# Kernel tuning notes

Hardware: AMD Instinct MI355X
Metric: run time of the kernel (lower is better)

Reference implementation:

```python
import jax, jax.numpy as jnp
import numpy as np


def setup_inputs() -> dict:
    key = jax.random.key(0)
    k1, k2, k3 = jax.random.split(key, 3)
    B, N, D = 8, 4096, 64
    q = jax.random.normal(k1, (B, N, D), dtype=jnp.float32)
    k = jax.random.normal(k2, (B, N, D), dtype=jnp.float32)
    v = jax.random.normal(k3, (B, N, D), dtype=jnp.float32)
    attn_mask = jnp.ones((B, N), dtype=jnp.int32)  # 1 = attend, 0 = padding
    return {"q": q, "k": k, "v": v, "attn_mask": attn_mask}


def reference(q, k, v, attn_mask):
    # q: [B, n_q, d], k/v: [B, n_k, d], attn_mask: [B, n_k]
    d = q.shape[-1]
    n_q, n_k = q.shape[1], k.shape[1]
    scale = jnp.sqrt(jnp.asarray(d, dtype=q.dtype))
    # [B, n_q, n_k] attention logits
    logits = jnp.einsum("bqd,bkd->bqk", q, k) / scale
    # causal (mask_future=True): tril keep-mask over (n_q, n_k)
    causal = jnp.tril(jnp.ones((n_q, n_k), dtype=bool))
    neg_inf = jnp.asarray(-jnp.inf, dtype=logits.dtype)
    logits = jnp.where(causal[None, :, :], logits, neg_inf)
    # padding mask broadcast over query dim: [B, 1, n_k]
    logits = jnp.where(attn_mask[:, None, :] == 0, neg_inf, logits)
    w = jax.nn.softmax(logits, axis=-1)
    return jnp.einsum("bqk,bkd->bqd", w, v)
```

## Files before the change

### kernel.cpp

```cpp
#include <hip/hip_runtime.h>


#define BATCH 8
#define SEQ   4096
#define DIM   64
#define QT    64
#define NKT   (SEQ / 64)

typedef __attribute__((ext_vector_type(8))) short bf16x8;
typedef __attribute__((ext_vector_type(4))) float f32x4;
typedef __attribute__((ext_vector_type(4))) unsigned u32x4;

__device__ inline short f2bf(float f) {
    unsigned u = __builtin_bit_cast(unsigned, f);
    u += 0x7FFFu + ((u >> 16) & 1u);
    return (short)(u >> 16);
}

__device__ inline unsigned pk2bf(float a, float b) {
    unsigned ua = __builtin_bit_cast(unsigned, a) + 0x8000u;
    unsigned ub = __builtin_bit_cast(unsigned, b) + 0x8000u;
    return __builtin_amdgcn_perm(ub, ua, 0x07060302u);
}

__device__ inline float fast_exp2(float x) {
#if __has_builtin(__builtin_amdgcn_exp2f)
    return __builtin_amdgcn_exp2f(x);
#else
    return exp2f(x);
#endif
}

__device__ inline void gl_lds16(const void* g, void* l) {
    __builtin_amdgcn_global_load_lds(
        (const __attribute__((address_space(1))) void*)g,
        (__attribute__((address_space(3))) void*)l, 16, 0, 0);
}

__device__ inline f32x4 ntl4(const float* p) {
    return __builtin_nontemporal_load((const f32x4*)p);
}

__global__ __launch_bounds__(256)
void prep_kv(const float* __restrict__ kg, const float* __restrict__ vg,
             const int* __restrict__ mg, short* __restrict__ kw,
             short* __restrict__ vw, float* __restrict__ mf) {
    const int tile = blockIdx.x;
    const float* kp = kg + (size_t)tile * 64 * DIM;
    const float* vp = vg + (size_t)tile * 64 * DIM;
    short* ko = kw + (size_t)tile * 4096;
    short* vo = vw + (size_t)tile * 4096;
    const int t = threadIdx.x;
    if (mf && t < 64) {
        const int* mp = mg + (size_t)tile * 64;
        mf[(size_t)tile * 64 + t] = mp[t] ? 0.0f : -1e30f;
    }
#pragma unroll
    for (int i = 0; i < 4; ++i) {
        const int flat = i * 256 + t;
        const int key = flat >> 4, d0 = (flat & 15) * 4;
        const f32x4 kv = ntl4(kp + (size_t)key * DIM + d0);
        uint2 kpk;
        kpk.x = pk2bf(kv[0], kv[1]); kpk.y = pk2bf(kv[2], kv[3]);
        *(uint2*)(ko + (((d0 >> 3) << 6) + key) * 8 + (d0 & 7)) = kpk;
        const f32x4 vv = ntl4(vp + (size_t)key * DIM + d0);
        const int vcell = ((key >> 5) << 2) | ((key >> 2) & 3);
        const int vj    = (((key >> 4) & 1) << 2) | (key & 3);
        vo[((vcell << 6) + d0 + 0) * 8 + vj] = f2bf(vv[0]);
        vo[((vcell << 6) + d0 + 1) * 8 + vj] = f2bf(vv[1]);
        vo[((vcell << 6) + d0 + 2) * 8 + vj] = f2bf(vv[2]);
        vo[((vcell << 6) + d0 + 3) * 8 + vj] = f2bf(vv[3]);
    }
}

__global__ __launch_bounds__(256, 4)
void attn_split4(const float* __restrict__ qg, float* __restrict__ og,
                 const short* __restrict__ kw, const short* __restrict__ vw,
                 const float* __restrict__ mf, float* __restrict__ opart,
                 float* __restrict__ lpart) {
    __shared__ __align__(16) char smem[32768];
    short* KbS = (short*)smem;
    float* OX = (float*)smem;
    float* LB = (float*)(smem + 16384);

    const int t    = threadIdx.x;
    const int w    = t >> 6;
    const int L    = t & 63;
    const int c15  = L & 15;
    const int quad = L >> 4;
    const int qgrp = w >> 1;
    const int kh   = w & 1;

    const int id  = blockIdx.x;
    const int b   = id & 7;
    const int r_  = id >> 3;
    const int j   = r_ & 31;
    const int ch  = r_ >> 5;
    const int nL  = 64 - j;
    const int qLt = 63 - j;

    const float* qp  = qg + (size_t)b * SEQ * DIM;
    const float* mb  = mf + (size_t)b * SEQ;
    const short* kwb = kw + (size_t)b * NKT * 4096;
    const short* vwb = vw + (size_t)b * NKT * 4096;
    float* osl = opart + (size_t)(b * 32 + j) * 12288;
    float* lsl = lpart + (size_t)(b * 32 + j) * 384;
    const float qscale = 0.125f * 1.44269504088896340736f;

    auto stage = [&](int bs, int kt) {
        const short* ks = kwb + (size_t)kt * 4096;
        const short* vs = vwb + (size_t)kt * 4096;
        const int off = w << 10;
        short* base = KbS + bs * 8192;
        gl_lds16(ks + off +       (L << 3), base + off);
        gl_lds16(ks + off + 512 + (L << 3), base + off + 512);
        gl_lds16(vs + off +       (L << 3), base + 4096 + off);
        gl_lds16(vs + off + 512 + (L << 3), base + 4096 + off + 512);
    };

    bf16x8 vones;
#pragma unroll
    for (int z = 0; z < 8; ++z) vones[z] = (short)0x3F80;

    int sqt[2], sk0[2], sk1[2], smode[2], sos[2], sls[2], nseg;
    sos[0] = sos[1] = 0; sls[0] = sls[1] = 0;
    if (ch == 0) {
        nseg = 1;
        sqt[0] = qLt; sk0[0] = 0;  sk1[0] = 16; smode[0] = 0; sls[0] = 0;
    } else if (ch == 1) {
        nseg = 1;
        sqt[0] = qLt; sk0[0] = 16; sk1[0] = 32; smode[0] = 1; sos[0] = 0; sls[0] = 1;
    } else if (ch == 2) {
        if (nL >= 48) {
            nseg = 1;
            sqt[0] = qLt; sk0[0] = 32; sk1[0] = 48; smode[0] = 1; sos[0] = 1; sls[0] = 2;
        } else {
            nseg = 2;
            sqt[0] = qLt; sk0[0] = 32; sk1[0] = nL;      smode[0] = 1; sos[0] = 1; sls[0] = 2;
            sqt[1] = j;   sk0[1] = 0;  sk1[1] = 48 - nL; smode[1] = 0; sls[1] = 4;
        }
    } else {
        if (nL > 48) {
            nseg = 2;
            sqt[0] = qLt; sk0[0] = 48; sk1[0] = nL;    smode[0] = 1; sos[0] = 2; sls[0] = 3;
            sqt[1] = j;   sk0[1] = 0;  sk1[1] = j + 1; smode[1] = 2;
        } else if (nL == 48) {
            nseg = 1;
            sqt[0] = j; sk0[0] = 0; sk1[0] = j + 1; smode[0] = 2;
        } else {
            nseg = 1;
            sqt[0] = j; sk0[0] = 48 - nL; sk1[0] = j + 1; smode[0] = 1; sos[0] = 2; sls[0] = 5;
        }
    }

    for (int seg = 0; seg < nseg; ++seg) {
        const int qt   = sqt[seg];
        const int kt0  = sk0[seg];
        const int kt1  = sk1[seg];
        const int mode = smode[seg];

        const int qbase = qt * QT;
        int qrow[2];
        qrow[0] = qbase + qgrp * 32 + c15;
        qrow[1] = qrow[0] + 16;

        bf16x8 Qf[2][2];
#pragma unroll
        for (int s = 0; s < 2; ++s) {
#pragma unroll
            for (int c = 0; c < 2; ++c) {
                const float* src = qp + (size_t)qrow[s] * DIM + c * 32 + quad * 8;
                float4 x = *(const float4*)(src);
                float4 y = *(const float4*)(src + 4);
                bf16x8 f;
                f[0] = f2bf(x.x * qscale); f[1] = f2bf(x.y * qscale);
                f[2] = f2bf(x.z * qscale); f[3] = f2bf(x.w * qscale);
                f[4] = f2bf(y.x * qscale); f[5] = f2bf(y.y * qscale);
                f[6] = f2bf(y.z * qscale); f[7] = f2bf(y.w * qscale);
                Qf[s][c] = f;
            }
        }
        asm volatile("" ::: "memory");

        f32x4 lacc[2];
        lacc[0] = (f32x4){0.f, 0.f, 0.f, 0.f};
        lacc[1] = (f32x4){0.f, 0.f, 0.f, 0.f};
        f32x4 Oacc[2][4];
#pragma unroll
        for (int s = 0; s < 2; ++s)
#pragma unroll
            for (int nb = 0; nb < 4; ++nb)
                Oacc[s][nb] = (f32x4){0.f, 0.f, 0.f, 0.f};

        stage(0, kt0);
        int cur = 0;
        const float* mrow = mb + (size_t)kt0 * 64 + (2 * kh) * 16 + quad * 4;

        for (int kt = kt0; kt < kt1; ++kt) {
            asm volatile("s_waitcnt vmcnt(0)" ::: "memory");
            __builtin_amdgcn_s_barrier();
            asm volatile("" ::: "memory");

            const float4 ma0 = *(const float4*)(mrow);
            const float4 ma1 = *(const float4*)(mrow + 16);
            mrow += 64;
            asm volatile("" ::: "memory");
            if (kt + 1 < kt1) stage(cur ^ 1, kt + 1);

            const short* Kt = KbS + cur * 8192;
            const short* Vt = Kt + 4096;
            cur ^= 1;

            f32x4 sacc[2][2];
#pragma unroll
            for (int s = 0; s < 2; ++s) {
                sacc[s][0] = (f32x4){ma0.x, ma0.y, ma0.z, ma0.w};
                sacc[s][1] = (f32x4){ma1.x, ma1.y, ma1.z, ma1.w};
            }
            __builtin_amdgcn_s_setprio(1);
#pragma unroll
            for (int c = 0; c < 2; ++c) {
#pragma unroll
                for (int i = 0; i < 2; ++i) {
                    bf16x8 kf = *(const bf16x8*)&Kt[(((quad + 4 * c) << 6) + (2 * kh + i) * 16 + c15) * 8];
#pragma unroll
                    for (int s = 0; s < 2; ++s)
                        sacc[s][i] = __builtin_amdgcn_mfma_f32_16x16x32_bf16(kf, Qf[s][c], sacc[s][i], 0, 0, 0);
                }
            }
            __builtin_amdgcn_s_setprio(0);

            const bool diag = (kt == qt);
            bf16x8 pf[2];
#pragma unroll
            for (int s = 0; s < 2; ++s) {
                unsigned pu[4];
#pragma unroll
                for (int i = 0; i < 2; ++i) {
                    float p[4];
#pragma unroll
                    for (int r = 0; r < 4; ++r) {
                        float sv = sacc[s][i][r];
                        if (diag) {
                            const int keyg = kt * 64 + (2 * kh + i) * 16 + quad * 4 + r;
                            if (keyg > qrow[s]) sv = -1e30f;
                        }
                        p[r] = fast_exp2(sv);
                    }
                    pu[2 * i]     = pk2bf(p[0], p[1]);
                    pu[2 * i + 1] = pk2bf(p[2], p[3]);
                }
                pf[s] = __builtin_bit_cast(bf16x8,
                    (u32x4){pu[0], pu[1], pu[2], pu[3]});
            }

            __builtin_amdgcn_s_setprio(1);
#pragma unroll
            for (int nb = 0; nb < 4; ++nb) {
                bf16x8 vf = *(const bf16x8*)&Vt[(((kh * 4 + quad) << 6) + nb * 16 + c15) * 8];
#pragma unroll
                for (int s = 0; s < 2; ++s)
                    Oacc[s][nb] = __builtin_amdgcn_mfma_f32_16x16x32_bf16(pf[s], vf, Oacc[s][nb], 0, 0, 0);
            }
            lacc[0] = __builtin_amdgcn_mfma_f32_16x16x32_bf16(pf[0], vones, lacc[0], 0, 0, 0);
            lacc[1] = __builtin_amdgcn_mfma_f32_16x16x32_bf16(pf[1], vones, lacc[1], 0, 0, 0);
            __builtin_amdgcn_s_setprio(0);
        }

        __syncthreads();
        if (kh == 1) {
#pragma unroll
            for (int s = 0; s < 2; ++s) {
#pragma unroll
                for (int r = 0; r < 4; ++r) {
                    const int rl = qgrp * 32 + s * 16 + quad * 4 + r;
#pragma unroll
                    for (int nb = 0; nb < 4; ++nb)
                        OX[rl * 64 + nb * 16 + c15] = Oacc[s][nb][r];
                    if (c15 == 0) LB[rl] = lacc[s][r];
                }
            }
        }
        __syncthreads();
        if (kh == 0) {
            float* dst = (mode == 1) ? osl + (size_t)sos[seg] * 4096
                                     : og + ((size_t)b * SEQ + qbase) * DIM;
#pragma unroll
            for (int s = 0; s < 2; ++s) {
#pragma unroll
                for (int r = 0; r < 4; ++r) {
                    const int rl = qgrp * 32 + s * 16 + quad * 4 + r;
                    const float lt = lacc[s][r] + LB[rl];
                    const float ir = (mode == 2) ? 1.0f / lt : 1.0f;
                    if (mode != 2 && c15 == 0)
                        lsl[sls[seg] * 64 + rl] = lt;
#pragma unroll
                    for (int nb = 0; nb < 4; ++nb)
                        dst[(size_t)rl * DIM + nb * 16 + c15] =
                            (Oacc[s][nb][r] + OX[rl * 64 + nb * 16 + c15]) * ir;
                }
            }
        }
        __syncthreads();
    }
}

__global__ __launch_bounds__(256)
void merge4(float* __restrict__ og, const float* __restrict__ opart,
            const float* __restrict__ lpart) {
    const int id = blockIdx.x;
    const int b = id & 7, j = id >> 3;
    const int nL = 64 - j, qLt = 63 - j;
    const float* os = opart + (size_t)(b * 32 + j) * 12288;
    const float* ls = lpart + (size_t)(b * 32 + j) * 384;
    const int t = threadIdx.x;
    const bool has3 = (nL > 48);

    float* opL = og + ((size_t)b * SEQ + (size_t)qLt * 64) * DIM;
#pragma unroll
    for (int i = 0; i < 4; ++i) {
        const int flat = i * 256 + t;
        const int row = flat >> 4;
        const int c4  = (flat & 15) * 4;
        float l = ls[row] + ls[64 + row] + ls[128 + row];
        if (has3) l += ls[192 + row];
        const float inv = 1.0f / l;
        const float4 a  = *(const float4*)(opL + (size_t)row * DIM + c4);
        const float4 p0 = *(const float4*)(os + (size_t)row * 64 + c4);
        const float4 p1 = *(const float4*)(os + 4096 + (size_t)row * 64 + c4);
        float sx = a.x + p0.x + p1.x;
        float sy = a.y + p0.y + p1.y;
        float sz = a.z + p0.z + p1.z;
        float sw = a.w + p0.w + p1.w;
        if (has3) {
            const float4 p2 = *(const float4*)(os + 8192 + (size_t)row * 64 + c4);
            sx += p2.x; sy += p2.y; sz += p2.z; sw += p2.w;
        }
        float4 r;
        r.x = sx * inv; r.y = sy * inv; r.z = sz * inv; r.w = sw * inv;
        *(float4*)(opL + (size_t)row * DIM + c4) = r;
    }

    if (nL < 48) {
        float* opS = og + ((size_t)b * SEQ + (size_t)j * 64) * DIM;
#pragma unroll
        for (int i = 0; i < 4; ++i) {
            const int flat = i * 256 + t;
            const int row = flat >> 4;
            const int c4  = (flat & 15) * 4;
            const float inv = 1.0f / (ls[256 + row] + ls[320 + row]);
            const float4 a  = *(const float4*)(opS + (size_t)row * DIM + c4);
            const float4 p2 = *(const float4*)(os + 8192 + (size_t)row * 64 + c4);
            float4 r;
            r.x = (a.x + p2.x) * inv;
            r.y = (a.y + p2.y) * inv;
            r.z = (a.z + p2.z) * inv;
            r.w = (a.w + p2.w) * inv;
            *(float4*)(opS + (size_t)row * DIM + c4) = r;
        }
    }
}

template <bool WS>
__global__ __launch_bounds__(512, 4)
void attn_fwd(const float* __restrict__ qg, const float* __restrict__ kg,
              const float* __restrict__ vg, const int* __restrict__ mg,
              float* __restrict__ og, const short* __restrict__ kw,
              const short* __restrict__ vw) {
    __shared__ __align__(16) char smem[59392];
    short* KbS = (short*)smem;
    short* VbS = (short*)(smem + 16384);
    float* Ml  = (float*)(smem + 43008);
    float* OX = (float*)smem;
    float* LB = (float*)(smem + 16384);

    const int t    = threadIdx.x;
    const int w    = t >> 6;
    const int L    = t & 63;
    const int c15  = L & 15;
    const int quad = L >> 4;
    const int qsub = w & 3;
    const int kh   = w >> 2;

    const int id = blockIdx.x;
    const int b  = id & 7;
    const int j  = id >> 3;
    const int qb = (j < 32) ? (63 - j) : (j - 32);
    const int qbase  = qb * QT;
    const int ntiles = qb + 1;

    const float* qp = qg + (size_t)b * SEQ * DIM;
    const float* kp = kg + (size_t)b * SEQ * DIM;
    const float* vp = vg + (size_t)b * SEQ * DIM;
    const int*   mp = mg + (size_t)b * SEQ;
    const short* kwb = WS ? kw + (size_t)b * NKT * 4096 : nullptr;
    const short* vwb = WS ? vw + (size_t)b * NKT * 4096 : nullptr;

    const int qrow = qbase + qsub * 16 + c15;
    const float qscale = 0.125f * 1.44269504088896340736f;

    bf16x8 Qf[2];
#pragma unroll
    for (int c = 0; c < 2; ++c) {
        const float* src = qp + (size_t)qrow * DIM + c * 32 + quad * 8;
        float4 x = *(const float4*)(src);
        float4 y = *(const float4*)(src + 4);
        bf16x8 f;
        f[0] = f2bf(x.x * qscale); f[1] = f2bf(x.y * qscale);
        f[2] = f2bf(x.z * qscale); f[3] = f2bf(x.w * qscale);
        f[4] = f2bf(y.x * qscale); f[5] = f2bf(y.y * qscale);
        f[6] = f2bf(y.z * qscale); f[7] = f2bf(y.w * qscale);
        Qf[c] = f;
    }

    auto stage = [&](int bs, int kt) {
        const short* ks = kwb + (size_t)kt * 4096;
        const short* vs = vwb + (size_t)kt * 4096;
        const int off = w << 9;
        gl_lds16(ks + off + (L << 3), KbS + bs * 4096 + off);
        gl_lds16(vs + off + (L << 3), VbS + bs * 4096 + off);
    };

    for (int i = t; i < ntiles * 64; i += 512)
        Ml[i] = mp[i] ? 0.0f : -1e30f;

    float lsum = 0.0f;
    f32x4 Oacc[4];
#pragma unroll
    for (int nb = 0; nb < 4; ++nb) Oacc[nb] = (f32x4){0.f, 0.f, 0.f, 0.f};

    if constexpr (WS) stage(0, 0);

    for (int kt = 0; kt < ntiles; ++kt) {
        const int cur = WS ? (kt & 1) : 0;

        if constexpr (!WS) {
            __syncthreads();
#pragma unroll
            for (int it = 0; it < 2; ++it) {
                const int flat = it * 512 + t;
                const int key = flat >> 4, d0 = (flat & 15) * 4;
                const float4 kv = *(const float4*)(kp + (size_t)(kt * 64 + key) * DIM + d0);
                uint2 kk;
                kk.x = pk2bf(kv.x, kv.y); kk.y = pk2bf(kv.z, kv.w);
                *(uint2*)&KbS[(((d0 >> 3) << 6) + key) * 8 + (d0 & 7)] = kk;
                const float4 vv = *(const float4*)(vp + (size_t)(kt * 64 + key) * DIM + d0);
                const int vcell = ((key >> 5) << 2) | ((key >> 2) & 3);
                const int vj    = (((key >> 4) & 1) << 2) | (key & 3);
                VbS[((vcell << 6) + d0 + 0) * 8 + vj] = f2bf(vv.x);
                VbS[((vcell << 6) + d0 + 1) * 8 + vj] = f2bf(vv.y);
                VbS[((vcell << 6) + d0 + 2) * 8 + vj] = f2bf(vv.z);
                VbS[((vcell << 6) + d0 + 3) * 8 + vj] = f2bf(vv.w);
            }
            __syncthreads();
        } else {
            __syncthreads();
            if (kt + 1 < ntiles) stage(cur ^ 1, kt + 1);
        }

        const short* Kt = KbS + cur * 4096;
        const short* Vt = VbS + cur * 4096;

        f32x4 sacc[2];
        sacc[0] = (f32x4){0.f, 0.f, 0.f, 0.f};
        sacc[1] = (f32x4){0.f, 0.f, 0.f, 0.f};
#pragma unroll
        for (int c = 0; c < 2; ++c) {
#pragma unroll
            for (int i = 0; i < 2; ++i) {
                bf16x8 kf = *(const bf16x8*)&Kt[(((quad + 4 * c) << 6) + (2 * kh + i) * 16 + c15) * 8];
                sacc[i] = __builtin_amdgcn_mfma_f32_16x16x32_bf16(kf, Qf[c], sacc[i], 0, 0, 0);
            }
        }

        const bool diag = (kt == ntiles - 1);
        unsigned pu[4];
#pragma unroll
        for (int i = 0; i < 2; ++i) {
            const int kb = 2 * kh + i;
            const float4 ma = *(const float4*)&Ml[kt * 64 + kb * 16 + quad * 4];
            const float mar[4] = {ma.x, ma.y, ma.z, ma.w};
            float p[4];
#pragma unroll
            for (int r = 0; r < 4; ++r) {
                float s = sacc[i][r] + mar[r];
                if (diag) {
                    const int keyg = kt * 64 + kb * 16 + quad * 4 + r;
                    if (keyg > qrow) s = -1e30f;
                }
                p[r] = fast_exp2(fminf(s, 80.0f));
                lsum += p[r];
            }
            pu[2 * i]     = pk2bf(p[0], p[1]);
            pu[2 * i + 1] = pk2bf(p[2], p[3]);
        }

        const bf16x8 pf = __builtin_bit_cast(bf16x8,
            (u32x4){pu[0], pu[1], pu[2], pu[3]});
#pragma unroll
        for (int nb = 0; nb < 4; ++nb) {
            bf16x8 vf = *(const bf16x8*)&Vt[(((kh * 4 + quad) << 6) + nb * 16 + c15) * 8];
            Oacc[nb] = __builtin_amdgcn_mfma_f32_16x16x32_bf16(pf, vf, Oacc[nb], 0, 0, 0);
        }
    }

    lsum += __shfl_xor(lsum, 16);
    lsum += __shfl_xor(lsum, 32);

    __syncthreads();
    if (w >= 4) {
        const int g = w & 3;
#pragma unroll
        for (int r = 0; r < 4; ++r) {
            const int q = quad * 4 + r;
#pragma unroll
            for (int nb = 0; nb < 4; ++nb)
                OX[(g * 16 + q) * 64 + nb * 16 + c15] = Oacc[nb][r];
        }
        if (quad == 0) LB[g * 16 + c15] = lsum;
    }
    __syncthreads();
    if (w < 4) {
        const float inv = 1.0f / (lsum + LB[w * 16 + c15]);
        float* op = og + (size_t)b * SEQ * DIM;
#pragma unroll
        for (int r = 0; r < 4; ++r) {
            const float ir = __shfl(inv, (L & 48) + ((L & 48) >> 2) + r);
            const int row = qbase + w * 16 + quad * 4 + r;
#pragma unroll
            for (int nb = 0; nb < 4; ++nb)
                op[(size_t)row * DIM + nb * 16 + c15] =
                    (Oacc[nb][r] + OX[(w * 16 + quad * 4 + r) * 64 + nb * 16 + c15]) * ir;
        }
    }
}

extern "C" void kernel_launch(void* const* d_in, const int* in_sizes, int n_in,
                              void* d_out, int out_size, void* d_ws, size_t ws_size,
                              hipStream_t stream) {
    (void)in_sizes; (void)n_in; (void)out_size;
    const float* q = (const float*)d_in[0];
    const float* k = (const float*)d_in[1];
    const float* v = (const float*)d_in[2];
    const int*   m = (const int*)d_in[3];
    float* o = (float*)d_out;

    const size_t kvB    = (size_t)BATCH * NKT * 4096 * sizeof(short);
    const size_t maddB  = (size_t)BATCH * SEQ * sizeof(float);
    const size_t opartB = (size_t)BATCH * 32 * 12288 * sizeof(float);
    const size_t lpartB = (size_t)BATCH * 32 * 384 * sizeof(float);
    const size_t need4  = 2 * kvB + maddB + opartB + lpartB;

    if (ws_size >= need4) {
        short* kw = (short*)d_ws;
        short* vw = kw + (size_t)BATCH * NKT * 4096;
        float* mf = (float*)((char*)d_ws + 2 * kvB);
        float* opart = (float*)((char*)d_ws + 2 * kvB + maddB);
        float* lpart = opart + (size_t)BATCH * 32 * 12288;
        prep_kv<<<dim3(BATCH * NKT), 256, 0, stream>>>(k, v, m, kw, vw, mf);
        attn_split4<<<dim3(1024), 256, 0, stream>>>(q, o, kw, vw, mf, opart, lpart);
        merge4<<<dim3(256), 256, 0, stream>>>(o, opart, lpart);
    } else if (ws_size >= 2 * kvB) {
        short* kw = (short*)d_ws;
        short* vw = kw + (size_t)BATCH * NKT * 4096;
        prep_kv<<<dim3(BATCH * NKT), 256, 0, stream>>>(k, v, m, kw, vw, nullptr);
        attn_fwd<true><<<dim3(512), 512, 0, stream>>>(q, k, v, m, o, kw, vw);
    } else {
        attn_fwd<false><<<dim3(512), 512, 0, stream>>>(q, k, v, m, o, nullptr, nullptr);
    }
}
```

Before: 122.3 us.

## Split paired causal query tiles into five uniform 13-tile key chunks

Replaces the four-chunk split (16 key tiles per chunk with special cases) for each paired long/short query tile with five uniform chunks of 13 key tiles. The attention kernel now launches 1280 blocks and always writes unnormalized partials plus row sums, and the merge kernel sums a variable number of partials for both query tiles and normalizes them. The aim is better load balance and more blocks to fill the GPU's compute units, at the cost of more partial-output traffic to the workspace and a heavier merge step.

```diff
diff --git a/kernel.cpp b/kernel.cpp
--- a/kernel.cpp
+++ b/kernel.cpp
@@ -73,8 +73,8 @@
     }
 }
 
-__global__ __launch_bounds__(256, 4)
-void attn_split4(const float* __restrict__ qg, float* __restrict__ og,
+__global__ __launch_bounds__(256, 5)
+void attn_split5(const float* __restrict__ qg, float* __restrict__ og,
                  const short* __restrict__ kw, const short* __restrict__ vw,
                  const float* __restrict__ mf, float* __restrict__ opart,
                  float* __restrict__ lpart) {
@@ -103,8 +103,8 @@
     const float* mb  = mf + (size_t)b * SEQ;
     const short* kwb = kw + (size_t)b * NKT * 4096;
     const short* vwb = vw + (size_t)b * NKT * 4096;
-    float* osl = opart + (size_t)(b * 32 + j) * 12288;
-    float* lsl = lpart + (size_t)(b * 32 + j) * 384;
+    float* osl = opart + (size_t)(b * 32 + j) * 24576;
+    float* lsl = lpart + (size_t)(b * 32 + j) * 512;
     const float qscale = 0.125f * 1.44269504088896340736f;
 
     auto stage = [&](int bs, int kt) {
@@ -122,42 +122,32 @@
 #pragma unroll
     for (int z = 0; z < 8; ++z) vones[z] = (short)0x3F80;
 
-    int sqt[2], sk0[2], sk1[2], smode[2], sos[2], sls[2], nseg;
-    sos[0] = sos[1] = 0; sls[0] = sls[1] = 0;
-    if (ch == 0) {
-        nseg = 1;
-        sqt[0] = qLt; sk0[0] = 0;  sk1[0] = 16; smode[0] = 0; sls[0] = 0;
-    } else if (ch == 1) {
-        nseg = 1;
-        sqt[0] = qLt; sk0[0] = 16; sk1[0] = 32; smode[0] = 1; sos[0] = 0; sls[0] = 1;
-    } else if (ch == 2) {
-        if (nL >= 48) {
-            nseg = 1;
-            sqt[0] = qLt; sk0[0] = 32; sk1[0] = 48; smode[0] = 1; sos[0] = 1; sls[0] = 2;
-        } else {
-            nseg = 2;
-            sqt[0] = qLt; sk0[0] = 32; sk1[0] = nL;      smode[0] = 1; sos[0] = 1; sls[0] = 2;
-            sqt[1] = j;   sk0[1] = 0;  sk1[1] = 48 - nL; smode[1] = 0; sls[1] = 4;
-        }
-    } else {
-        if (nL > 48) {
-            nseg = 2;
-            sqt[0] = qLt; sk0[0] = 48; sk1[0] = nL;    smode[0] = 1; sos[0] = 2; sls[0] = 3;
-            sqt[1] = j;   sk0[1] = 0;  sk1[1] = j + 1; smode[1] = 2;
-        } else if (nL == 48) {
-            nseg = 1;
-            sqt[0] = j; sk0[0] = 0; sk1[0] = j + 1; smode[0] = 2;
-        } else {
-            nseg = 1;
-            sqt[0] = j; sk0[0] = 48 - nL; sk1[0] = j + 1; smode[0] = 1; sos[0] = 2; sls[0] = 5;
-        }
+    int sqt[2], sk0[2], sk1[2], sog[2], sos[2], sls[2], nseg = 0;
+    const int p0 = 13 * ch, p1 = p0 + 13;
+    const int cS = nL / 13;
+    if (p0 < nL) {
+        sqt[nseg] = qLt;
+        sk0[nseg] = p0;
+        sk1[nseg] = (p1 < nL ? p1 : nL);
+        sog[nseg] = (ch == 0);
+        sos[nseg] = ch - 1;
+        sls[nseg] = ch;
+        ++nseg;
+    }
+    if (p1 > nL) {
+        sqt[nseg] = j;
+        sk0[nseg] = (p0 > nL ? p0 : nL) - nL;
+        sk1[nseg] = p1 - nL;
+        sog[nseg] = (ch == cS);
+        sos[nseg] = 4 + (ch - cS - 1);
+        sls[nseg] = 5 + (ch - cS);
+        ++nseg;
     }
 
     for (int seg = 0; seg < nseg; ++seg) {
-        const int qt   = sqt[seg];
-        const int kt0  = sk0[seg];
-        const int kt1  = sk1[seg];
-        const int mode = smode[seg];
+        const int qt  = sqt[seg];
+        const int kt0 = sk0[seg];
+        const int kt1 = sk1[seg];
 
         const int qbase = qt * QT;
         int qrow[2];
@@ -283,21 +273,20 @@
         }
         __syncthreads();
         if (kh == 0) {
-            float* dst = (mode == 1) ? osl + (size_t)sos[seg] * 4096
-                                     : og + ((size_t)b * SEQ + qbase) * DIM;
+            float* dst = sog[seg] ? og + ((size_t)b * SEQ + qbase) * DIM
+                                  : osl + (size_t)sos[seg] * 4096;
 #pragma unroll
             for (int s = 0; s < 2; ++s) {
 #pragma unroll
                 for (int r = 0; r < 4; ++r) {
                     const int rl = qgrp * 32 + s * 16 + quad * 4 + r;
                     const float lt = lacc[s][r] + LB[rl];
-                    const float ir = (mode == 2) ? 1.0f / lt : 1.0f;
-                    if (mode != 2 && c15 == 0)
+                    if (c15 == 0)
                         lsl[sls[seg] * 64 + rl] = lt;
 #pragma unroll
                     for (int nb = 0; nb < 4; ++nb)
                         dst[(size_t)rl * DIM + nb * 16 + c15] =
-                            (Oacc[s][nb][r] + OX[rl * 64 + nb * 16 + c15]) * ir;
+                            Oacc[s][nb][r] + OX[rl * 64 + nb * 16 + c15];
                 }
             }
         }
@@ -306,58 +295,46 @@
 }
 
 __global__ __launch_bounds__(256)
-void merge4(float* __restrict__ og, const float* __restrict__ opart,
+void merge5(float* __restrict__ og, const float* __restrict__ opart,
             const float* __restrict__ lpart) {
     const int id = blockIdx.x;
     const int b = id & 7, j = id >> 3;
     const int nL = 64 - j, qLt = 63 - j;
-    const float* os = opart + (size_t)(b * 32 + j) * 12288;
-    const float* ls = lpart + (size_t)(b * 32 + j) * 384;
+    const int cL = (nL - 1) / 13;
+    const int cS = nL / 13;
+    const float* os = opart + (size_t)(b * 32 + j) * 24576;
+    const float* ls = lpart + (size_t)(b * 32 + j) * 512;
     const int t = threadIdx.x;
-    const bool has3 = (nL > 48);
 
     float* opL = og + ((size_t)b * SEQ + (size_t)qLt * 64) * DIM;
+    float* opS = og + ((size_t)b * SEQ + (size_t)j * 64) * DIM;
 #pragma unroll
     for (int i = 0; i < 4; ++i) {
         const int flat = i * 256 + t;
         const int row = flat >> 4;
         const int c4  = (flat & 15) * 4;
-        float l = ls[row] + ls[64 + row] + ls[128 + row];
-        if (has3) l += ls[192 + row];
+
+        float l = 0.f;
+        for (int c = 0; c <= cL; ++c) l += ls[c * 64 + row];
+        float4 s = *(const float4*)(opL + (size_t)row * DIM + c4);
+        for (int c = 1; c <= cL; ++c) {
+            const float4 p = *(const float4*)(os + (size_t)(c - 1) * 4096 + row * 64 + c4);
+            s.x += p.x; s.y += p.y; s.z += p.z; s.w += p.w;
+        }
         const float inv = 1.0f / l;
-        const float4 a  = *(const float4*)(opL + (size_t)row * DIM + c4);
-        const float4 p0 = *(const float4*)(os + (size_t)row * 64 + c4);
-        const float4 p1 = *(const float4*)(os + 4096 + (size_t)row * 64 + c4);
-        float sx = a.x + p0.x + p1.x;
-        float sy = a.y + p0.y + p1.y;
-        float sz = a.z + p0.z + p1.z;
-        float sw = a.w + p0.w + p1.w;
-        if (has3) {
-            const float4 p2 = *(const float4*)(os + 8192 + (size_t)row * 64 + c4);
-            sx += p2.x; sy += p2.y; sz += p2.z; sw += p2.w;
-        }
-        float4 r;
-        r.x = sx * inv; r.y = sy * inv; r.z = sz * inv; r.w = sw * inv;
-        *(float4*)(opL + (size_t)row * DIM + c4) = r;
-    }
-
-    if (nL < 48) {
-        float* opS = og + ((size_t)b * SEQ + (size_t)j * 64) * DIM;
-#pragma unroll
-        for (int i = 0; i < 4; ++i) {
-            const int flat = i * 256 + t;
-            const int row = flat >> 4;
-            const int c4  = (flat & 15) * 4;
-            const float inv = 1.0f / (ls[256 + row] + ls[320 + row]);
-            const float4 a  = *(const float4*)(opS + (size_t)row * DIM + c4);
-            const float4 p2 = *(const float4*)(os + 8192 + (size_t)row * 64 + c4);
-            float4 r;
-            r.x = (a.x + p2.x) * inv;
-            r.y = (a.y + p2.y) * inv;
-            r.z = (a.z + p2.z) * inv;
-            r.w = (a.w + p2.w) * inv;
-            *(float4*)(opS + (size_t)row * DIM + c4) = r;
-        }
+        s.x *= inv; s.y *= inv; s.z *= inv; s.w *= inv;
+        *(float4*)(opL + (size_t)row * DIM + c4) = s;
+
+        float l2 = 0.f;
+        for (int c = cS; c <= 4; ++c) l2 += ls[(5 + c - cS) * 64 + row];
+        float4 s2 = *(const float4*)(opS + (size_t)row * DIM + c4);
+        for (int c = cS + 1; c <= 4; ++c) {
+            const float4 p = *(const float4*)(os + (size_t)(4 + c - cS - 1) * 4096 + row * 64 + c4);
+            s2.x += p.x; s2.y += p.y; s2.z += p.z; s2.w += p.w;
+        }
+        const float inv2 = 1.0f / l2;
+        s2.x *= inv2; s2.y *= inv2; s2.z *= inv2; s2.w *= inv2;
+        *(float4*)(opS + (size_t)row * DIM + c4) = s2;
     }
 }
 
@@ -547,19 +524,19 @@
 
     const size_t kvB    = (size_t)BATCH * NKT * 4096 * sizeof(short);
     const size_t maddB  = (size_t)BATCH * SEQ * sizeof(float);
-    const size_t opartB = (size_t)BATCH * 32 * 12288 * sizeof(float);
-    const size_t lpartB = (size_t)BATCH * 32 * 384 * sizeof(float);
-    const size_t need4  = 2 * kvB + maddB + opartB + lpartB;
-
-    if (ws_size >= need4) {
+    const size_t opartB = (size_t)BATCH * 32 * 24576 * sizeof(float);
+    const size_t lpartB = (size_t)BATCH * 32 * 512 * sizeof(float);
+    const size_t need5  = 2 * kvB + maddB + opartB + lpartB;
+
+    if (ws_size >= need5) {
         short* kw = (short*)d_ws;
         short* vw = kw + (size_t)BATCH * NKT * 4096;
         float* mf = (float*)((char*)d_ws + 2 * kvB);
         float* opart = (float*)((char*)d_ws + 2 * kvB + maddB);
-        float* lpart = opart + (size_t)BATCH * 32 * 12288;
+        float* lpart = opart + (size_t)BATCH * 32 * 24576;
         prep_kv<<<dim3(BATCH * NKT), 256, 0, stream>>>(k, v, m, kw, vw, mf);
-        attn_split4<<<dim3(1024), 256, 0, stream>>>(q, o, kw, vw, mf, opart, lpart);
-        merge4<<<dim3(256), 256, 0, stream>>>(o, opart, lpart);
+        attn_split5<<<dim3(1280), 256, 0, stream>>>(q, o, kw, vw, mf, opart, lpart);
+        merge5<<<dim3(256), 256, 0, stream>>>(o, opart, lpart);
     } else if (ws_size >= 2 * kvB) {
         short* kw = (short*)d_ws;
         short* vw = kw + (size_t)BATCH * NKT * 4096;
```

Measured after the change: 169.4 us. +38.5%, slower.
